# Kernel tuning notes

Hardware: AMD Instinct MI355X
Metric: run time of the kernel (lower is better)

Reference implementation:

```python
import jax, jax.numpy as jnp
import numpy as np

ALPHA = 0.2  # leaky-relu negative slope


def setup_inputs() -> dict:
    key = jax.random.key(0)
    k1, k2, k3, k4 = jax.random.split(key, 4)
    bs, L, D, Fin, Fout = 4, 20000, 16, 128, 128
    x = jax.random.normal(k1, (bs, L, Fin), dtype=jnp.float32)
    adj = jax.random.randint(k2, (bs, L, D), 0, L, dtype=jnp.int64)
    # xavier_normal-ish init for W [Fin, Fout] and a [2*Fout, 1]
    W = jax.random.normal(k3, (Fin, Fout), dtype=jnp.float32) * (1.414 * np.sqrt(2.0 / (Fin + Fout))).astype(np.float32)
    a = jax.random.normal(k4, (2 * Fout, 1), dtype=jnp.float32) * (1.414 * np.sqrt(2.0 / (2 * Fout + 1))).astype(np.float32)
    return {"x": x, "adj": adj, "W": W, "a": a}


def reference(x, adj, W, a):
    Fout = W.shape[1]
    # gather fixed-degree neighbor features: [bs, L, D, Fin]
    nbr = jax.vmap(lambda xb, ab: xb[ab])(x, adj)
    h = jnp.matmul(nbr, W)  # [bs, L, D, Fout]
    # a is applied to cat([h_neighbor, h_center]); split it instead of concatenating
    a1 = a[:Fout, 0]
    a2 = a[Fout:, 0]
    # h[:, :, 0, :] is the center node (first neighbor slot, repeat_interleave in torch)
    e = jnp.einsum('bldf,f->bld', h, a1) + jnp.einsum('blf,f->bl', h[:, :, 0, :], a2)[..., None]
    attn = jax.nn.softmax(jax.nn.leaky_relu(e, ALPHA), axis=-1)  # softmax over D
    out = jnp.einsum('bld,bldf->blf', attn, h)  # weighted aggregate [bs, L, Fout]
    return jax.nn.elu(out)  # concat=True branch
```

## Files before the change

### kernel.cpp

```cpp
#include <hip/hip_runtime.h>
#include <hip/hip_bf16.h>

#define LSEQ 20000
#define DEG  16
#define F    128
#define FP   136
#define ALPHA 0.2f

typedef __bf16 bf16x8 __attribute__((ext_vector_type(8)));
typedef float  f32x4  __attribute__((ext_vector_type(4)));

__global__ __launch_bounds__(256) void gat_wt(const float* __restrict__ W,
                                              const float* __restrict__ a,
                                              __hip_bfloat16* __restrict__ wt,
                                              float* __restrict__ wa)
{
    const int t = blockIdx.x * 256 + threadIdx.x;
    for (int i = t; i < F * F; i += 16 * 256) {
        const int k = i >> 7, n = i & (F - 1);
        wt[n * F + k] = __float2bfloat16(W[i]);
    }
    if (blockIdx.x == 0 && threadIdx.x < F) {
        const int k = threadIdx.x;
        float acc1 = 0.f, acc2 = 0.f;
        for (int n = 0; n < F; ++n) {
            const float w = W[k * F + n];
            acc1 = fmaf(w, a[n],     acc1);
            acc2 = fmaf(w, a[F + n], acc2);
        }
        wa[k]     = acc1;
        wa[F + k] = acc2;
    }
}

__global__ __launch_bounds__(256) void gat_gemm(const float* __restrict__ x,
                                                const __hip_bfloat16* __restrict__ wt,
                                                const float* __restrict__ wa,
                                                __hip_bfloat16* __restrict__ y16,
                                                float* __restrict__ s1,
                                                float* __restrict__ s2)
{
    __shared__ __hip_bfloat16 wl[F][FP];

    const int t    = threadIdx.x;
    const int lane = t & 63;
    const int wid  = t >> 6;
    const int i0   = (blockIdx.x * 4 + wid) * 16;
    const int m    = lane & 15;
    const int q    = lane >> 4;

    {
        const uint4* wg = reinterpret_cast<const uint4*>(wt);
        #pragma unroll
        for (int i = 0; i < 8; ++i) {
            const int g   = t + 256 * i;
            const int row = g >> 4;
            const int c8  = g & 15;
            *reinterpret_cast<uint4*>(&wl[row][c8 * 8]) = wg[g];
        }
    }

    const float* xr = x + (size_t)(i0 + m) * F + q * 8;
    float4 xf[8];
    #pragma unroll
    for (int kt = 0; kt < 4; ++kt) {
        xf[2*kt]   = *reinterpret_cast<const float4*>(xr + kt * 32);
        xf[2*kt+1] = *reinterpret_cast<const float4*>(xr + kt * 32 + 4);
    }

    float p1 = 0.f, p2 = 0.f;
    {
        const float* w1p = wa + q * 8;
        const float* w2p = wa + F + q * 8;
        #pragma unroll
        for (int kt = 0; kt < 4; ++kt) {
            const float4 u0 = *reinterpret_cast<const float4*>(w1p + kt * 32);
            const float4 u1 = *reinterpret_cast<const float4*>(w1p + kt * 32 + 4);
            const float4 v0 = *reinterpret_cast<const float4*>(w2p + kt * 32);
            const float4 v1 = *reinterpret_cast<const float4*>(w2p + kt * 32 + 4);
            const float4 xa = xf[2*kt], xb = xf[2*kt+1];
            p1 = fmaf(xa.x,u0.x,p1); p1 = fmaf(xa.y,u0.y,p1);
            p1 = fmaf(xa.z,u0.z,p1); p1 = fmaf(xa.w,u0.w,p1);
            p1 = fmaf(xb.x,u1.x,p1); p1 = fmaf(xb.y,u1.y,p1);
            p1 = fmaf(xb.z,u1.z,p1); p1 = fmaf(xb.w,u1.w,p1);
            p2 = fmaf(xa.x,v0.x,p2); p2 = fmaf(xa.y,v0.y,p2);
            p2 = fmaf(xa.z,v0.z,p2); p2 = fmaf(xa.w,v0.w,p2);
            p2 = fmaf(xb.x,v1.x,p2); p2 = fmaf(xb.y,v1.y,p2);
            p2 = fmaf(xb.z,v1.z,p2); p2 = fmaf(xb.w,v1.w,p2);
        }
    }
    p1 += __shfl_xor(p1, 16); p1 += __shfl_xor(p1, 32);
    p2 += __shfl_xor(p2, 16); p2 += __shfl_xor(p2, 32);
    if (lane < 16) {
        s1[i0 + m] = p1;
        s2[i0 + m] = p2;
    }

    bf16x8 bfr[4];
    #pragma unroll
    for (int kt = 0; kt < 4; ++kt) {
        const float4 qa = xf[2*kt], qb = xf[2*kt+1];
        bf16x8 f;
        f[0] = (__bf16)qa.x; f[1] = (__bf16)qa.y; f[2] = (__bf16)qa.z; f[3] = (__bf16)qa.w;
        f[4] = (__bf16)qb.x; f[5] = (__bf16)qb.y; f[6] = (__bf16)qb.z; f[7] = (__bf16)qb.w;
        bfr[kt] = f;
    }

    __syncthreads();

    #pragma unroll
    for (int ct = 0; ct < 8; ++ct) {
        union { uint4 u; bf16x8 v; } afr[4];
        const __hip_bfloat16* wrow = &wl[ct * 16 + m][q * 8];
        #pragma unroll
        for (int kt = 0; kt < 4; ++kt)
            afr[kt].u = *reinterpret_cast<const uint4*>(wrow + kt * 32);

        f32x4 acc = {0.f, 0.f, 0.f, 0.f};
        #pragma unroll
        for (int kt = 0; kt < 4; ++kt)
            acc = __builtin_amdgcn_mfma_f32_16x16x32_bf16(afr[kt].v, bfr[kt], acc, 0, 0, 0);

        union { uint2 u; __hip_bfloat162 h[2]; } pk;
        pk.h[0] = __float22bfloat162_rn(make_float2(acc[0], acc[1]));
        pk.h[1] = __float22bfloat162_rn(make_float2(acc[2], acc[3]));
        *reinterpret_cast<uint2*>(y16 + (size_t)(i0 + m) * F + ct * 16 + q * 4) = pk.u;
    }
}

__global__ __launch_bounds__(256) void gat_attn(const int* __restrict__ adj,
                                                const __hip_bfloat16* __restrict__ y16,
                                                const float* __restrict__ s1,
                                                const float* __restrict__ s2,
                                                float* __restrict__ out)
{
    const int lane  = threadIdx.x & 63;
    const int wid   = threadIdx.x >> 6;
    const int x8    = blockIdx.x & 7;
    const int j     = blockIdx.x >> 3;
    const int batch = x8 >> 1;
    const int grp   = j * 2 + (x8 & 1);
    const int base  = batch * LSEQ;
    const int g0    = base + grp * 16 + wid * 4;

    const int av = adj[(size_t)g0 * DEG + lane];

    const float sv = s1[base + av];
    const int d = lane & 15;
    float s2l = (d == 0) ? s2[base + av] : 0.f;
    const float s2v = __shfl(s2l, lane & 48);
    const float e = sv + s2v;
    const float t = e > 0.f ? e : ALPHA * e;

    float m = t;
    #pragma unroll
    for (int off = 1; off < 16; off <<= 1) m = fmaxf(m, __shfl_xor(m, off));
    const float w = __expf(t - m);
    float p = w;
    #pragma unroll
    for (int off = 1; off < 16; off <<= 1) p += __shfl_xor(p, off);
    const float attn = w / p;

    #pragma unroll
    for (int n = 0; n < 4; n += 2) {
        unsigned int v0[DEG], v1[DEG];
        #pragma unroll
        for (int dd = 0; dd < DEG; ++dd) {
            const int i0 = __builtin_amdgcn_readlane(av, n * 16 + dd);
            v0[dd] = reinterpret_cast<const unsigned int*>(
                         y16 + ((size_t)(base + i0) << 7))[lane];
        }
        #pragma unroll
        for (int dd = 0; dd < DEG; ++dd) {
            const int i1 = __builtin_amdgcn_readlane(av, (n + 1) * 16 + dd);
            v1[dd] = reinterpret_cast<const unsigned int*>(
                         y16 + ((size_t)(base + i1) << 7))[lane];
        }

        float ax0 = 0.f, ay0 = 0.f, ax1 = 0.f, ay1 = 0.f;
        #pragma unroll
        for (int dd = 0; dd < DEG; ++dd) {
            const float ad0 = __uint_as_float(__builtin_amdgcn_readlane(
                                  __float_as_uint(attn), n * 16 + dd));
            union { unsigned int u; __hip_bfloat162 h; } c0; c0.u = v0[dd];
            const float2 f0 = __bfloat1622float2(c0.h);
            ax0 = fmaf(ad0, f0.x, ax0); ay0 = fmaf(ad0, f0.y, ay0);

            const float ad1 = __uint_as_float(__builtin_amdgcn_readlane(
                                  __float_as_uint(attn), (n + 1) * 16 + dd));
            union { unsigned int u; __hip_bfloat162 h; } c1; c1.u = v1[dd];
            const float2 f1 = __bfloat1622float2(c1.h);
            ax1 = fmaf(ad1, f1.x, ax1); ay1 = fmaf(ad1, f1.y, ay1);
        }
        const float ox0 = ax0 > 0.f ? ax0 : __expf(ax0) - 1.f;
        const float oy0 = ay0 > 0.f ? ay0 : __expf(ay0) - 1.f;
        *reinterpret_cast<float2*>(out + (size_t)(g0 + n) * F + lane * 2)
            = make_float2(ox0, oy0);
        const float ox1 = ax1 > 0.f ? ax1 : __expf(ax1) - 1.f;
        const float oy1 = ay1 > 0.f ? ay1 : __expf(ay1) - 1.f;
        *reinterpret_cast<float2*>(out + (size_t)(g0 + n + 1) * F + lane * 2)
            = make_float2(ox1, oy1);
    }
}

extern "C" void kernel_launch(void* const* d_in, const int* in_sizes, int n_in,
                              void* d_out, int out_size, void* d_ws, size_t ws_size,
                              hipStream_t stream) {
    const float* x   = (const float*)d_in[0];
    const int*   adj = (const int*)d_in[1];
    const float* W   = (const float*)d_in[2];
    const float* a   = (const float*)d_in[3];
    float* out = (float*)d_out;

    const int BL = in_sizes[0] / F;

    __hip_bfloat16* y16 = (__hip_bfloat16*)d_ws;
    float* s1 = (float*)((char*)d_ws + (size_t)BL * F * sizeof(__hip_bfloat16));
    float* s2 = s1 + BL;
    __hip_bfloat16* wt = (__hip_bfloat16*)(s2 + BL);
    float* wa = (float*)(wt + F * F);

    gat_wt  <<<16, 256, 0, stream>>>(W, a, wt, wa);
    gat_gemm<<<BL / 64, 256, 0, stream>>>(x, wt, wa, y16, s1, s2);
    gat_attn<<<BL / 16, 256, 0, stream>>>(adj, y16, s1, s2, out);
}
```

Baseline: 134.2 us.

## Vectorize neighbor gathers to 16-byte loads and XOR-swizzle the GEMM weight tile

```diff
diff --git a/kernel.cpp b/kernel.cpp
--- a/kernel.cpp
+++ b/kernel.cpp
@@ -4,11 +4,14 @@
 #define LSEQ 20000
 #define DEG  16
 #define F    128
-#define FP   136
 #define ALPHA 0.2f
 
 typedef __bf16 bf16x8 __attribute__((ext_vector_type(8)));
 typedef float  f32x4  __attribute__((ext_vector_type(4)));
+
+__device__ __forceinline__ float bf_lo(unsigned int u) { return __uint_as_float(u << 16); }
+__device__ __forceinline__ float bf_hi(unsigned int u) { return __uint_as_float(u & 0xffff0000u); }
+__device__ __forceinline__ float elu_f(float v) { return v > 0.f ? v : __expf(v) - 1.f; }
 
 __global__ __launch_bounds__(256) void gat_wt(const float* __restrict__ W,
                                               const float* __restrict__ a,
@@ -33,14 +36,14 @@
     }
 }
 
-__global__ __launch_bounds__(256) void gat_gemm(const float* __restrict__ x,
-                                                const __hip_bfloat16* __restrict__ wt,
-                                                const float* __restrict__ wa,
-                                                __hip_bfloat16* __restrict__ y16,
-                                                float* __restrict__ s1,
-                                                float* __restrict__ s2)
+__global__ __launch_bounds__(256, 5) void gat_gemm(const float* __restrict__ x,
+                                                   const __hip_bfloat16* __restrict__ wt,
+                                                   const float* __restrict__ wa,
+                                                   __hip_bfloat16* __restrict__ y16,
+                                                   float* __restrict__ s1,
+                                                   float* __restrict__ s2)
 {
-    __shared__ __hip_bfloat16 wl[F][FP];
+    __shared__ __hip_bfloat16 wl[F][F];
 
     const int t    = threadIdx.x;
     const int lane = t & 63;
@@ -56,7 +59,7 @@
             const int g   = t + 256 * i;
             const int row = g >> 4;
             const int c8  = g & 15;
-            *reinterpret_cast<uint4*>(&wl[row][c8 * 8]) = wg[g];
+            *reinterpret_cast<uint4*>(&wl[row][((c8 ^ (row & 7)) * 8)]) = wg[g];
         }
     }
 
@@ -111,10 +114,11 @@
     #pragma unroll
     for (int ct = 0; ct < 8; ++ct) {
         union { uint4 u; bf16x8 v; } afr[4];
-        const __hip_bfloat16* wrow = &wl[ct * 16 + m][q * 8];
+        const int row = ct * 16 + m;
         #pragma unroll
         for (int kt = 0; kt < 4; ++kt)
-            afr[kt].u = *reinterpret_cast<const uint4*>(wrow + kt * 32);
+            afr[kt].u = *reinterpret_cast<const uint4*>(
+                            &wl[row][(((kt * 4 + q) ^ (m & 7)) * 8)]);
 
         f32x4 acc = {0.f, 0.f, 0.f, 0.f};
         #pragma unroll
@@ -128,11 +132,11 @@
     }
 }
 
-__global__ __launch_bounds__(256) void gat_attn(const int* __restrict__ adj,
-                                                const __hip_bfloat16* __restrict__ y16,
-                                                const float* __restrict__ s1,
-                                                const float* __restrict__ s2,
-                                                float* __restrict__ out)
+__global__ __launch_bounds__(256, 4) void gat_attn(const int* __restrict__ adj,
+                                                   const __hip_bfloat16* __restrict__ y16,
+                                                   const float* __restrict__ s1,
+                                                   const float* __restrict__ s2,
+                                                   float* __restrict__ out)
 {
     const int lane  = threadIdx.x & 63;
     const int wid   = threadIdx.x >> 6;
@@ -142,65 +146,75 @@
     const int grp   = j * 2 + (x8 & 1);
     const int base  = batch * LSEQ;
     const int g0    = base + grp * 16 + wid * 4;
+    const int d     = lane & 15;
+    const int g16   = lane & 48;
 
     const int av = adj[(size_t)g0 * DEG + lane];
 
     const float sv = s1[base + av];
-    const int d = lane & 15;
     float s2l = (d == 0) ? s2[base + av] : 0.f;
-    const float s2v = __shfl(s2l, lane & 48);
+    const float s2v = __shfl(s2l, g16);
     const float e = sv + s2v;
     const float t = e > 0.f ? e : ALPHA * e;
 
-    float m = t;
-    #pragma unroll
-    for (int off = 1; off < 16; off <<= 1) m = fmaxf(m, __shfl_xor(m, off));
-    const float w = __expf(t - m);
+    float mx = t;
+    #pragma unroll
+    for (int off = 1; off < 16; off <<= 1) mx = fmaxf(mx, __shfl_xor(mx, off));
+    const float w = __expf(t - mx);
     float p = w;
     #pragma unroll
     for (int off = 1; off < 16; off <<= 1) p += __shfl_xor(p, off);
     const float attn = w / p;
 
-    #pragma unroll
-    for (int n = 0; n < 4; n += 2) {
-        unsigned int v0[DEG], v1[DEG];
-        #pragma unroll
-        for (int dd = 0; dd < DEG; ++dd) {
-            const int i0 = __builtin_amdgcn_readlane(av, n * 16 + dd);
-            v0[dd] = reinterpret_cast<const unsigned int*>(
-                         y16 + ((size_t)(base + i0) << 7))[lane];
-        }
-        #pragma unroll
-        for (int dd = 0; dd < DEG; ++dd) {
-            const int i1 = __builtin_amdgcn_readlane(av, (n + 1) * 16 + dd);
-            v1[dd] = reinterpret_cast<const unsigned int*>(
-                         y16 + ((size_t)(base + i1) << 7))[lane];
-        }
-
-        float ax0 = 0.f, ay0 = 0.f, ax1 = 0.f, ay1 = 0.f;
-        #pragma unroll
-        for (int dd = 0; dd < DEG; ++dd) {
-            const float ad0 = __uint_as_float(__builtin_amdgcn_readlane(
-                                  __float_as_uint(attn), n * 16 + dd));
-            union { unsigned int u; __hip_bfloat162 h; } c0; c0.u = v0[dd];
-            const float2 f0 = __bfloat1622float2(c0.h);
-            ax0 = fmaf(ad0, f0.x, ax0); ay0 = fmaf(ad0, f0.y, ay0);
-
-            const float ad1 = __uint_as_float(__builtin_amdgcn_readlane(
-                                  __float_as_uint(attn), (n + 1) * 16 + dd));
-            union { unsigned int u; __hip_bfloat162 h; } c1; c1.u = v1[dd];
-            const float2 f1 = __bfloat1622float2(c1.h);
-            ax1 = fmaf(ad1, f1.x, ax1); ay1 = fmaf(ad1, f1.y, ay1);
-        }
-        const float ox0 = ax0 > 0.f ? ax0 : __expf(ax0) - 1.f;
-        const float oy0 = ay0 > 0.f ? ay0 : __expf(ay0) - 1.f;
-        *reinterpret_cast<float2*>(out + (size_t)(g0 + n) * F + lane * 2)
-            = make_float2(ox0, oy0);
-        const float ox1 = ax1 > 0.f ? ax1 : __expf(ax1) - 1.f;
-        const float oy1 = ay1 > 0.f ? ay1 : __expf(ay1) - 1.f;
-        *reinterpret_cast<float2*>(out + (size_t)(g0 + n + 1) * F + lane * 2)
-            = make_float2(ox1, oy1);
-    }
+    const char* yb = reinterpret_cast<const char*>(y16 + ((size_t)base << 7)) + d * 16;
+    float acc[8] = {0.f, 0.f, 0.f, 0.f, 0.f, 0.f, 0.f, 0.f};
+
+    uint4 va[8], vb[8];
+    #pragma unroll
+    for (int k = 0; k < 8; ++k) {
+        const int r = __shfl(av, g16 + k);
+        va[k] = *reinterpret_cast<const uint4*>(yb + ((size_t)r << 8));
+    }
+    #pragma unroll
+    for (int k = 0; k < 8; ++k) {
+        const int r = __shfl(av, g16 + 8 + k);
+        vb[k] = *reinterpret_cast<const uint4*>(yb + ((size_t)r << 8));
+    }
+
+    #pragma unroll
+    for (int k = 0; k < 8; ++k) {
+        const float wk = __shfl(attn, g16 + k);
+        const uint4 v = va[k];
+        acc[0] = fmaf(wk, bf_lo(v.x), acc[0]);
+        acc[1] = fmaf(wk, bf_hi(v.x), acc[1]);
+        acc[2] = fmaf(wk, bf_lo(v.y), acc[2]);
+        acc[3] = fmaf(wk, bf_hi(v.y), acc[3]);
+        acc[4] = fmaf(wk, bf_lo(v.z), acc[4]);
+        acc[5] = fmaf(wk, bf_hi(v.z), acc[5]);
+        acc[6] = fmaf(wk, bf_lo(v.w), acc[6]);
+        acc[7] = fmaf(wk, bf_hi(v.w), acc[7]);
+    }
+    #pragma unroll
+    for (int k = 0; k < 8; ++k) {
+        const float wk = __shfl(attn, g16 + 8 + k);
+        const uint4 v = vb[k];
+        acc[0] = fmaf(wk, bf_lo(v.x), acc[0]);
+        acc[1] = fmaf(wk, bf_hi(v.x), acc[1]);
+        acc[2] = fmaf(wk, bf_lo(v.y), acc[2]);
+        acc[3] = fmaf(wk, bf_hi(v.y), acc[3]);
+        acc[4] = fmaf(wk, bf_lo(v.z), acc[4]);
+        acc[5] = fmaf(wk, bf_hi(v.z), acc[5]);
+        acc[6] = fmaf(wk, bf_lo(v.w), acc[6]);
+        acc[7] = fmaf(wk, bf_hi(v.w), acc[7]);
+    }
+
+    float* op = out + (size_t)(g0 + (lane >> 4)) * F + d * 8;
+    const float4 o0 = make_float4(elu_f(acc[0]), elu_f(acc[1]),
+                                  elu_f(acc[2]), elu_f(acc[3]));
+    const float4 o1 = make_float4(elu_f(acc[4]), elu_f(acc[5]),
+                                  elu_f(acc[6]), elu_f(acc[7]));
+    *reinterpret_cast<float4*>(op)     = o0;
+    *reinterpret_cast<float4*>(op + 4) = o1;
 }
 
 extern "C" void kernel_launch(void* const* d_in, const int* in_sizes, int n_in,
```

Result: slower. 137.6 us (+2.5%).
